# Kernel optimization log

Hardware: AMD Instinct MI355X
Metric: run time of the kernel (lower is better)

The kernel has to match this reference:

```python
import jax, jax.numpy as jnp
import numpy as np

B, NV, NQ = 32, 512, 128
V_DIM, Q_DIM, H_DIM, K, H_OUT = 2048, 1024, 512, 3, 8
HK = H_DIM * K  # 1536


def setup_inputs() -> dict:
    key = jax.random.key(0)
    ks = jax.random.split(key, 8)
    s_v = 1.0 / np.sqrt(V_DIM)
    s_q = 1.0 / np.sqrt(Q_DIM)
    return {
        "v": jax.random.normal(ks[0], (B, NV, V_DIM), dtype=jnp.float32),
        "q": jax.random.normal(ks[1], (B, NQ, Q_DIM), dtype=jnp.float32),
        "Wv": jax.random.uniform(ks[2], (HK, V_DIM), jnp.float32, -s_v, s_v),
        "bv": jax.random.uniform(ks[3], (HK,), jnp.float32, -s_v, s_v),
        "Wq": jax.random.uniform(ks[4], (HK, Q_DIM), jnp.float32, -s_q, s_q),
        "bq": jax.random.uniform(ks[5], (HK,), jnp.float32, -s_q, s_q),
        "h_mat": jax.random.normal(ks[6], (H_OUT, HK), dtype=jnp.float32),
        "h_bias": jax.random.normal(ks[7], (H_OUT,), dtype=jnp.float32),
    }


def reference(v, q, Wv, bv, Wq, bq, h_mat, h_bias):
    # FCNet (single weight-norm Linear + ReLU); dropout is identity at eval.
    v_ = jax.nn.relu(jnp.einsum('bvd,kd->bvk', v, Wv) + bv)  # (B, NV, HK)
    q_ = jax.nn.relu(jnp.einsum('bqd,kd->bqk', q, Wq) + bq)  # (B, NQ, HK)
    # Three-way low-rank bilinear contraction over the rank dim k.
    logits = jnp.einsum('hk,bvk,bqk->bhvq', h_mat, v_, q_)
    return logits + h_bias[None, :, None, None]
```

## Files before the change

kernel.cpp:

```cpp
#include <hip/hip_runtime.h>


typedef _Float16 h8 __attribute__((ext_vector_type(8)));
typedef float f32x4 __attribute__((ext_vector_type(4)));

#define B_   32
#define NV_  512
#define NQ_  128
#define VD_  2048
#define QD_  1024
#define HK_  1536
#define HO_  8

__device__ __forceinline__ void gload_lds16(const void* g, void* l) {
  __builtin_amdgcn_global_load_lds(
      (const __attribute__((address_space(1))) void*)g,
      (__attribute__((address_space(3))) void*)l, 16, 0, 0);
}

__global__ __launch_bounds__(256) void cvt_all(
    const float* __restrict__ v, const float* __restrict__ q,
    const float* __restrict__ Wv, const float* __restrict__ Wq,
    const float* __restrict__ hm,
    _Float16* __restrict__ v16, _Float16* __restrict__ q16,
    _Float16* __restrict__ Wv16, _Float16* __restrict__ Wq16,
    _Float16* __restrict__ h16) {
  int i = blockIdx.x * blockDim.x + threadIdx.x;
  const float* src;
  _Float16* dst;
  if (i < 4194304)      { src = v;  dst = v16; }
  else if (i < 4718592) { src = q;  dst = q16;  i -= 4194304; }
  else if (i < 5111808) { src = Wv; dst = Wv16; i -= 4718592; }
  else if (i < 5308416) { src = Wq; dst = Wq16; i -= 5111808; }
  else                  { src = hm; dst = h16;  i -= 5308416; }
  const float4* p = (const float4*)src;
  float4 a = p[i * 2], b = p[i * 2 + 1];
  h8 o;
  o[0] = (_Float16)a.x; o[1] = (_Float16)a.y; o[2] = (_Float16)a.z; o[3] = (_Float16)a.w;
  o[4] = (_Float16)b.x; o[5] = (_Float16)b.y; o[6] = (_Float16)b.z; o[7] = (_Float16)b.w;
  ((h8*)dst)[i] = o;
}

template <int KTOT>
__global__ __launch_bounds__(256, 3) void gemm_m97_relu_f16(
    const _Float16* __restrict__ A, const _Float16* __restrict__ Bw,
    const float* __restrict__ bias, _Float16* __restrict__ out, int N) {
  __shared__ __align__(16) _Float16 As[2][128 * 32];
  __shared__ __align__(16) _Float16 Bs[2][128 * 32];

  const int t = threadIdx.x;
  const int lane = t & 63;
  const int wave = t >> 6;
  const int wm = wave >> 1, wn = wave & 1;
  const int bcol = blockIdx.x * 128;
  const int brow = blockIdx.y * 128;

  const int scol = ((t & 3) ^ ((t >> 3) & 3)) * 8;
  const _Float16* Ab = A + (size_t)(brow + (t >> 2)) * KTOT + scol;
  const _Float16* Bb = Bw + (size_t)(bcol + (t >> 2)) * KTOT + scol;

  f32x4 acc[4][4] = {};

  for (int kt = 0; kt < KTOT / 64; ++kt) {
    __syncthreads();
#pragma unroll
    for (int kk = 0; kk < 2; ++kk) {
      gload_lds16(Ab + kt * 64 + kk * 32, &As[kk][t * 8]);
      gload_lds16(Ab + (size_t)64 * KTOT + kt * 64 + kk * 32, &As[kk][2048 + t * 8]);
      gload_lds16(Bb + kt * 64 + kk * 32, &Bs[kk][t * 8]);
      gload_lds16(Bb + (size_t)64 * KTOT + kt * 64 + kk * 32, &Bs[kk][2048 + t * 8]);
    }
    asm volatile("s_waitcnt vmcnt(0)" ::: "memory");
    __syncthreads();
#pragma unroll
    for (int kk = 0; kk < 2; ++kk) {
      h8 af[4], bf[4];
#pragma unroll
      for (int m = 0; m < 4; ++m) {
        const int row = wm * 64 + m * 16 + (lane & 15);
        af[m] = *(const h8*)&As[kk][row * 32 + ((lane >> 4) ^ ((row >> 1) & 3)) * 8];
      }
#pragma unroll
      for (int n = 0; n < 4; ++n) {
        const int row = wn * 64 + n * 16 + (lane & 15);
        bf[n] = *(const h8*)&Bs[kk][row * 32 + ((lane >> 4) ^ ((row >> 1) & 3)) * 8];
      }
#pragma unroll
      for (int m = 0; m < 4; ++m)
#pragma unroll
        for (int n = 0; n < 4; ++n)
          acc[m][n] = __builtin_amdgcn_mfma_f32_16x16x32_f16(af[m], bf[n], acc[m][n], 0, 0, 0);
    }
  }

#pragma unroll
  for (int m = 0; m < 4; ++m)
#pragma unroll
    for (int n = 0; n < 4; ++n) {
      const int col = bcol + wn * 64 + n * 16 + (lane & 15);
      const float bb = bias[col];
#pragma unroll
      for (int r = 0; r < 4; ++r) {
        const int row = brow + wm * 64 + m * 16 + (lane >> 4) * 4 + r;
        float val = acc[m][n][r] + bb;
        out[(size_t)row * N + col] = (_Float16)(val > 0.f ? val : 0.f);
      }
    }
}

__global__ __launch_bounds__(256, 3) void bilinear_m97_f16(
    const _Float16* __restrict__ vh, const _Float16* __restrict__ qh,
    const _Float16* __restrict__ h16, const float* __restrict__ hbias,
    float* __restrict__ out) {
  __shared__ __align__(16) _Float16 As[2][128 * 32];
  __shared__ __align__(16) _Float16 Bs[2][128 * 32];
  __shared__ __align__(16) _Float16 hl[HK_];

  const int t = threadIdx.x;
  const int lane = t & 63;
  const int wave = t >> 6;
  const int wm = wave >> 1, wn = wave & 1;
  const int mt = blockIdx.x;
  const int bh = blockIdx.y;
  const int b = bh >> 3, h = bh & 7;

  const int scol = ((t & 3) ^ ((t >> 3) & 3)) * 8;
  const _Float16* Ab = vh + ((size_t)b * NV_ + mt * 128 + (t >> 2)) * HK_ + scol;
  const _Float16* Qb = qh + (size_t)b * NQ_ * HK_;

  for (int i = t; i < HK_ / 8; i += 256)
    *(h8*)&hl[i * 8] = *(const h8*)&h16[(size_t)h * HK_ + i * 8];

  const int qrow = t >> 2;
  const int qs = t & 3;

  f32x4 acc[4][4] = {};

  for (int kt = 0; kt < HK_ / 64; ++kt) {
    __syncthreads();
#pragma unroll
    for (int kk = 0; kk < 2; ++kk) {
      gload_lds16(Ab + kt * 64 + kk * 32, &As[kk][t * 8]);
      gload_lds16(Ab + (size_t)64 * HK_ + kt * 64 + kk * 32, &As[kk][2048 + t * 8]);
    }
#pragma unroll
    for (int u = 0; u < 2; ++u) {
      const int row = u * 64 + qrow;
#pragma unroll
      for (int kk = 0; kk < 2; ++kk) {
        const int col = kt * 64 + kk * 32 + qs * 8;
        h8 qv = *(const h8*)&Qb[(size_t)row * HK_ + col];
        h8 hv = *(const h8*)&hl[col];
        *(h8*)&Bs[kk][row * 32 + (qs ^ ((row >> 1) & 3)) * 8] = qv * hv;
      }
    }
    asm volatile("s_waitcnt vmcnt(0)" ::: "memory");
    __syncthreads();
#pragma unroll
    for (int kk = 0; kk < 2; ++kk) {
      h8 af[4], bf[4];
#pragma unroll
      for (int m = 0; m < 4; ++m) {
        const int row = wm * 64 + m * 16 + (lane & 15);
        af[m] = *(const h8*)&As[kk][row * 32 + ((lane >> 4) ^ ((row >> 1) & 3)) * 8];
      }
#pragma unroll
      for (int n = 0; n < 4; ++n) {
        const int row = wn * 64 + n * 16 + (lane & 15);
        bf[n] = *(const h8*)&Bs[kk][row * 32 + ((lane >> 4) ^ ((row >> 1) & 3)) * 8];
      }
#pragma unroll
      for (int m = 0; m < 4; ++m)
#pragma unroll
        for (int n = 0; n < 4; ++n)
          acc[m][n] = __builtin_amdgcn_mfma_f32_16x16x32_f16(af[m], bf[n], acc[m][n], 0, 0, 0);
    }
  }

  const float bb = hbias[h];
  float* O = out + ((size_t)bh * NV_ + (size_t)mt * 128) * NQ_;
#pragma unroll
  for (int m = 0; m < 4; ++m)
#pragma unroll
    for (int n = 0; n < 4; ++n)
#pragma unroll
      for (int r = 0; r < 4; ++r) {
        const int row = wm * 64 + m * 16 + (lane >> 4) * 4 + r;
        const int col = wn * 64 + n * 16 + (lane & 15);
        O[(size_t)row * NQ_ + col] = acc[m][n][r] + bb;
      }
}

extern "C" void kernel_launch(void* const* d_in, const int* in_sizes, int n_in,
                              void* d_out, int out_size, void* d_ws,
                              size_t ws_size, hipStream_t stream) {
  const float* v = (const float*)d_in[0];
  const float* q = (const float*)d_in[1];
  const float* Wv = (const float*)d_in[2];
  const float* bv = (const float*)d_in[3];
  const float* Wq = (const float*)d_in[4];
  const float* bq = (const float*)d_in[5];
  const float* hmat = (const float*)d_in[6];
  const float* hbias = (const float*)d_in[7];

  if (ws_size < 147873792u) return;

  char* ws = (char*)d_ws;
  _Float16* v16 = (_Float16*)(ws);
  _Float16* q16 = (_Float16*)(ws + 67108864);
  _Float16* Wv16 = (_Float16*)(ws + 75497472);
  _Float16* Wq16 = (_Float16*)(ws + 81788928);
  _Float16* vh = (_Float16*)(ws + 84934656);
  _Float16* qh = (_Float16*)(ws + 135266304);
  _Float16* h16 = (_Float16*)(ws + 147849216);

  cvt_all<<<dim3(20742), 256, 0, stream>>>(v, q, Wv, Wq, hmat,
                                           v16, q16, Wv16, Wq16, h16);

  gemm_m97_relu_f16<VD_><<<dim3(HK_ / 128, 16384 / 128), 256, 0, stream>>>(
      v16, Wv16, bv, vh, HK_);
  gemm_m97_relu_f16<QD_><<<dim3(HK_ / 128, 4096 / 128), 256, 0, stream>>>(
      q16, Wq16, bq, qh, HK_);

  bilinear_m97_f16<<<dim3(NV_ / 128, B_ * HO_), 256, 0, stream>>>(
      vh, qh, h16, hbias, (float*)d_out);
}
```

Before: 247.3 us.

## Use 256x256 tiled, double-buffered pipelined GEMM for the v projection

Adds a new 512-thread GEMM kernel with 256x256 output tiles, each wave computing 128x64, and uses it for the large v-projection GEMM. Global-to-LDS loads are double-buffered two k-steps ahead, interleaved with MFMA phases using barriers and s_setprio to overlap memory with compute. The aim is more data reuse per tile and hiding load latency that the single-buffered 128x128 kernel exposes. The cost is higher LDS (128KB) and register use, which limits occupancy, and a smaller grid (6x64 blocks).

```diff
diff --git a/kernel.cpp b/kernel.cpp
--- a/kernel.cpp
+++ b/kernel.cpp
@@ -11,6 +11,9 @@
 #define QD_  1024
 #define HK_  1536
 #define HO_  8
+
+#define SBAR()   asm volatile("s_barrier" ::: "memory")
+#define WAITV(n) asm volatile("s_waitcnt vmcnt(" #n ")" ::: "memory")
 
 __device__ __forceinline__ void gload_lds16(const void* g, void* l) {
   __builtin_amdgcn_global_load_lds(
@@ -42,6 +45,106 @@
 }
 
 template <int KTOT>
+__global__ __launch_bounds__(512, 2) void gemm256_relu_f16(
+    const _Float16* __restrict__ A, const _Float16* __restrict__ Bw,
+    const float* __restrict__ bias, _Float16* __restrict__ out, int N) {
+  __shared__ __align__(16) _Float16 Asl[2][2][256 * 32];
+  __shared__ __align__(16) _Float16 Bsl[2][2][256 * 32];
+
+  const int t = threadIdx.x;
+  const int lane = t & 63;
+  const int wave = t >> 6;
+  const int wm = wave >> 2;
+  const int wn = wave & 3;
+
+  const int bcol = blockIdx.x * 256;
+  const int brow = blockIdx.y * 256;
+
+  const int srow = t >> 2;
+  const int scol = ((t & 3) ^ ((t >> 3) & 3)) * 8;
+
+  constexpr int NT = KTOT / 64;
+  f32x4 acc[8][4] = {};
+
+  auto stgA = [&](int kt, int kk) {
+    const int bi = kt & 1;
+    const _Float16* s = A + (size_t)(brow + srow) * KTOT + kt * 64 + kk * 32 + scol;
+    gload_lds16(s, &Asl[bi][kk][t * 8]);
+    gload_lds16(s + (size_t)128 * KTOT, &Asl[bi][kk][4096 + t * 8]);
+  };
+  auto stgB = [&](int kt, int kk) {
+    const int bi = kt & 1;
+    const _Float16* s = Bw + (size_t)(bcol + srow) * KTOT + kt * 64 + kk * 32 + scol;
+    gload_lds16(s, &Bsl[bi][kk][t * 8]);
+    gload_lds16(s + (size_t)128 * KTOT, &Bsl[bi][kk][4096 + t * 8]);
+  };
+
+  h8 af[4], bf[4];
+  auto rdA = [&](int bi, int kk, int mh) {
+#pragma unroll
+    for (int m = 0; m < 4; ++m) {
+      const int row = wm * 128 + mh * 64 + m * 16 + (lane & 15);
+      af[m] = *(const h8*)&Asl[bi][kk][row * 32 + (((lane >> 4) ^ ((row >> 1) & 3)) * 8)];
+    }
+  };
+  auto rdB = [&](int bi, int kk) {
+#pragma unroll
+    for (int n = 0; n < 4; ++n) {
+      const int row = wn * 64 + n * 16 + (lane & 15);
+      bf[n] = *(const h8*)&Bsl[bi][kk][row * 32 + (((lane >> 4) ^ ((row >> 1) & 3)) * 8)];
+    }
+  };
+  auto mfma16 = [&](int mh) {
+    __builtin_amdgcn_s_setprio(1);
+#pragma unroll
+    for (int m = 0; m < 4; ++m)
+#pragma unroll
+      for (int n = 0; n < 4; ++n)
+        acc[mh * 4 + m][n] =
+            __builtin_amdgcn_mfma_f32_16x16x32_f16(af[m], bf[n], acc[mh * 4 + m][n], 0, 0, 0);
+    __builtin_amdgcn_s_setprio(0);
+  };
+
+  stgA(0, 0); stgB(0, 0); stgA(0, 1); stgB(0, 1);
+  stgA(1, 0); stgB(1, 0); stgA(1, 1); stgB(1, 1);
+  WAITV(8); SBAR();
+
+  for (int kt = 0; kt < NT; ++kt) {
+    const int bi = kt & 1;
+    rdA(bi, 0, 0); rdB(bi, 0);
+    SBAR(); mfma16(0); SBAR();
+    rdA(bi, 0, 1);
+    SBAR(); mfma16(1); SBAR();
+    rdA(bi, 1, 0); rdB(bi, 1);
+    if (kt + 2 < NT) { stgA(kt + 2, 0); stgB(kt + 2, 0); }
+    SBAR(); mfma16(0); SBAR();
+    rdA(bi, 1, 1);
+    SBAR(); mfma16(1); SBAR();
+    if (kt + 2 < NT) {
+      stgA(kt + 2, 1); stgB(kt + 2, 1);
+      WAITV(8); SBAR();
+    } else if (kt + 1 < NT) {
+      WAITV(0); SBAR();
+    }
+  }
+
+#pragma unroll
+  for (int mi = 0; mi < 8; ++mi) {
+#pragma unroll
+    for (int n = 0; n < 4; ++n) {
+      const int col = bcol + wn * 64 + n * 16 + (lane & 15);
+      const float bb = bias[col];
+#pragma unroll
+      for (int r = 0; r < 4; ++r) {
+        const int row = brow + wm * 128 + mi * 16 + (lane >> 4) * 4 + r;
+        float val = acc[mi][n][r] + bb;
+        out[(size_t)row * N + col] = (_Float16)(val > 0.f ? val : 0.f);
+      }
+    }
+  }
+}
+
+template <int KTOT>
 __global__ __launch_bounds__(256, 3) void gemm_m97_relu_f16(
     const _Float16* __restrict__ A, const _Float16* __restrict__ Bw,
     const float* __restrict__ bias, _Float16* __restrict__ out, int N) {
@@ -217,7 +320,7 @@
   cvt_all<<<dim3(20742), 256, 0, stream>>>(v, q, Wv, Wq, hmat,
                                            v16, q16, Wv16, Wq16, h16);
 
-  gemm_m97_relu_f16<VD_><<<dim3(HK_ / 128, 16384 / 128), 256, 0, stream>>>(
+  gemm256_relu_f16<VD_><<<dim3(HK_ / 256, 16384 / 256), 512, 0, stream>>>(
       v16, Wv16, bv, vh, HK_);
   gemm_m97_relu_f16<QD_><<<dim3(HK_ / 128, 4096 / 128), 256, 0, stream>>>(
       q16, Wq16, bq, qh, HK_);
```

After: 272.8 us. 10.3% more time.
